# Kernel tuning notes

Measured on AMD Instinct MI355X. Metric: run time of the kernel, lower is better.

Reference implementation:

```python
import jax, jax.numpy as jnp
import numpy as np

B, T, D_MODEL = 1, 4096, 1024
H = 16
SEM_DIM, GEO_DIM, ATTN_DIM = 128, 256, 512
SEM_HD, GEO_HD, V_HD = SEM_DIM // H, GEO_DIM // H, ATTN_DIM // H
ROPE_BASE = 10000.0


def _split_heads(x, hd):
    # (B,T,H*hd) -> (B,H,T,hd)
    b, t, _ = x.shape
    return x.reshape(b, t, H, hd).transpose(0, 2, 1, 3)


def _rope(x, pos_offset, base=ROPE_BASE):
    # x: (B,H,T,rot) with rot == full geo head dim (rotate applies to first rot_dim;
    # here rot_dim == geo_head_dim so the whole vector rotates)
    rot = x.shape[-1]
    inv_freq = 1.0 / (base ** (jnp.arange(0, rot, 2, dtype=jnp.float32) / rot))
    t = jnp.arange(pos_offset, pos_offset + x.shape[2], dtype=jnp.float32)
    freqs = t[:, None] * inv_freq[None, :]            # (T, rot/2)
    cos = jnp.cos(freqs).astype(x.dtype)[None, None]  # (1,1,T,rot/2)
    sin = jnp.sin(freqs).astype(x.dtype)[None, None]
    x1, x2 = x[..., : rot // 2], x[..., rot // 2 :]
    return jnp.concatenate([x1 * cos - x2 * sin, x1 * sin + x2 * cos], axis=-1)


def setup_inputs() -> dict:
    key = jax.random.key(0)
    ks = jax.random.split(key, 8)
    s = lambda fan_in: 1.0 / np.sqrt(fan_in)
    inp = {
        "x": jax.random.normal(ks[0], (B, T, D_MODEL), dtype=jnp.float32),
        "q_sem_w": jax.random.uniform(ks[1], (SEM_DIM, D_MODEL), jnp.float32, -s(D_MODEL), s(D_MODEL)),
        "k_sem_w": jax.random.uniform(ks[2], (SEM_DIM, D_MODEL), jnp.float32, -s(D_MODEL), s(D_MODEL)),
        "q_geo_w": jax.random.uniform(ks[3], (GEO_DIM, D_MODEL), jnp.float32, -s(D_MODEL), s(D_MODEL)),
        "k_geo_w": jax.random.uniform(ks[4], (GEO_DIM, D_MODEL), jnp.float32, -s(D_MODEL), s(D_MODEL)),
        "v_w": jax.random.uniform(ks[5], (ATTN_DIM, D_MODEL), jnp.float32, -s(D_MODEL), s(D_MODEL)),
        "out_w": jax.random.uniform(ks[6], (D_MODEL, ATTN_DIM), jnp.float32, -s(ATTN_DIM), s(ATTN_DIM)),
        "logit_scale": jnp.zeros((H,), dtype=jnp.float32),
        "attn_mask": jnp.tril(jnp.ones((T, T), dtype=bool)),  # causal: True = attend
        "pos_offset": 0,
    }
    return inp


def reference(x, q_sem_w, k_sem_w, q_geo_w, k_geo_w, v_w, out_w, logit_scale, attn_mask, pos_offset):
    dt = x.dtype
    ninf = jnp.finfo(dt).min
    # decoupled projections
    qs = _split_heads(x @ q_sem_w.T, SEM_HD)   # (B,H,T,sem_hd)
    ksem = _split_heads(x @ k_sem_w.T, SEM_HD)
    qg = _split_heads(x @ q_geo_w.T, GEO_HD)   # (B,H,T,geo_hd)
    kg = _split_heads(x @ k_geo_w.T, GEO_HD)
    v = _split_heads(x @ v_w.T, V_HD)          # (B,H,T,v_hd)
    # RoPE on geometric stream only
    qg = _rope(qg, pos_offset)
    kg = _rope(kg, pos_offset)
    # combined scores, scaled as one concatenated QK dot product
    scale = 1.0 / np.sqrt(SEM_HD + GEO_HD)
    scores = (jnp.einsum("bhtd,bhsd->bhts", qs, ksem)
              + jnp.einsum("bhtd,bhsd->bhts", qg, kg)) * scale
    # learned per-head temperature
    scores = scores * jnp.exp(logit_scale)[None, :, None, None]
    scores = jnp.where(attn_mask[None, None], scores, ninf)
    attn = jax.nn.softmax(scores, axis=-1)
    out = jnp.einsum("bhts,bhsd->bhtd", attn, v)       # (B,H,T,v_hd)
    out = out.transpose(0, 2, 1, 3).reshape(B, T, ATTN_DIM)
    return out @ out_w.T                                # (B,T,d_model)
```

## Files before the change

kernel.cpp:

```cpp
#include <hip/hip_runtime.h>
#include <hip/hip_bf16.h>

typedef __attribute__((ext_vector_type(8))) short short8;
typedef __attribute__((ext_vector_type(4))) short short4v;
typedef __attribute__((ext_vector_type(4))) float f32x4;

#define TT 4096
#define DM 1024
#define NH 16
#define NPROJ 1280
#define DATTN 512

static __device__ __forceinline__ short f2bf(float f) {
  __hip_bfloat16 h = __float2bfloat16(f);
  return *reinterpret_cast<short*>(&h);
}
static __device__ __forceinline__ float bf2f(__hip_bfloat16 h) { return __bfloat162float(h); }
static __device__ __forceinline__ float bfs2f(short s) {
  __hip_bfloat16 h = *reinterpret_cast<__hip_bfloat16*>(&s);
  return __bfloat162float(h);
}

#define NB_X   (TT * DM / 4 / 256)
#define NB_OW  (DM * DATTN / 4 / 256)
#define NB_WC  (NPROJ * DM / 4 / 256)
__global__ __launch_bounds__(256) void k_prep(const float* __restrict__ x,
    const float* __restrict__ ow, const float* __restrict__ qs, const float* __restrict__ ks,
    const float* __restrict__ qg, const float* __restrict__ kg, const float* __restrict__ vw,
    __hip_bfloat16* __restrict__ Xbf, __hip_bfloat16* __restrict__ OW,
    __hip_bfloat16* __restrict__ Wcat) {
  const int b = blockIdx.x;
  if (b < NB_X) {
    const int i = b * 256 + threadIdx.x;
    float4 v = reinterpret_cast<const float4*>(x)[i];
    short4v o;
    o[0] = f2bf(v.x); o[1] = f2bf(v.y); o[2] = f2bf(v.z); o[3] = f2bf(v.w);
    reinterpret_cast<short4v*>(Xbf)[i] = o;
  } else if (b < NB_X + NB_OW) {
    const int i = (b - NB_X) * 256 + threadIdx.x;
    float4 v = reinterpret_cast<const float4*>(ow)[i];
    short4v o;
    o[0] = f2bf(v.x); o[1] = f2bf(v.y); o[2] = f2bf(v.z); o[3] = f2bf(v.w);
    reinterpret_cast<short4v*>(OW)[i] = o;
  } else {
    const int i = (b - NB_X - NB_OW) * 256 + threadIdx.x;
    const int idx = i * 4;
    const int row = idx >> 10;
    const int col = idx & 1023;
    const float* src;
    if (row < 128)      src = qs + (size_t)row * DM;
    else if (row < 256) src = ks + (size_t)(row - 128) * DM;
    else if (row < 512) src = qg + (size_t)(row - 256) * DM;
    else if (row < 768) src = kg + (size_t)(row - 512) * DM;
    else                src = vw + (size_t)(row - 768) * DM;
    float4 v = *reinterpret_cast<const float4*>(src + col);
    short4v o;
    o[0] = f2bf(v.x); o[1] = f2bf(v.y); o[2] = f2bf(v.z); o[3] = f2bf(v.w);
    *reinterpret_cast<short4v*>(Wcat + idx) = o;
  }
}

template<int OUT_BF16>
__global__ __launch_bounds__(256) void k_gemm_bt(const __hip_bfloat16* __restrict__ A,
    const __hip_bfloat16* __restrict__ B, void* __restrict__ Cv, int M, int N, int K) {
  __shared__ alignas(16) __hip_bfloat16 lA[64 * 32];
  __shared__ alignas(16) __hip_bfloat16 lB[128 * 32];
  const int tid = threadIdx.x;
  const int lane = tid & 63;
  const int wid = tid >> 6;
  const int m0 = blockIdx.x * 64, n0 = blockIdx.y * 128;
  const int wm = (wid >> 1) * 32, wn = (wid & 1) * 64;
  const int srow = tid >> 2;
  const int scol = (tid & 3) * 8;
  const int fr = lane & 15, fk = (lane >> 4) * 8;
  f32x4 acc[2][4];
  const f32x4 zz = {0.f, 0.f, 0.f, 0.f};
#pragma unroll
  for (int m = 0; m < 2; ++m)
#pragma unroll
    for (int n = 0; n < 4; ++n) acc[m][n] = zz;

  for (int kt = 0; kt < K; kt += 32) {
    __syncthreads();
    {
      const __hip_bfloat16* ga0 = A + (size_t)(m0 + srow) * K + kt + scol;
      const __hip_bfloat16* gb0 = B + (size_t)(n0 + srow) * K + kt + scol;
      const __hip_bfloat16* gb1 = B + (size_t)(n0 + 64 + srow) * K + kt + scol;
      __builtin_amdgcn_global_load_lds((const __attribute__((address_space(1))) void*)ga0,
          (__attribute__((address_space(3))) void*)(lA + srow * 32 + scol), 16, 0, 0);
      __builtin_amdgcn_global_load_lds((const __attribute__((address_space(1))) void*)gb0,
          (__attribute__((address_space(3))) void*)(lB + srow * 32 + scol), 16, 0, 0);
      __builtin_amdgcn_global_load_lds((const __attribute__((address_space(1))) void*)gb1,
          (__attribute__((address_space(3))) void*)(lB + (64 + srow) * 32 + scol), 16, 0, 0);
    }
    __syncthreads();
    short8 af[2], bfr[4];
#pragma unroll
    for (int m = 0; m < 2; ++m)
      af[m] = *reinterpret_cast<const short8*>(lA + (wm + m * 16 + fr) * 32 + fk);
#pragma unroll
    for (int n = 0; n < 4; ++n)
      bfr[n] = *reinterpret_cast<const short8*>(lB + (wn + n * 16 + fr) * 32 + fk);
#pragma unroll
    for (int m = 0; m < 2; ++m)
#pragma unroll
      for (int n = 0; n < 4; ++n)
        acc[m][n] = __builtin_amdgcn_mfma_f32_16x16x32_bf16(af[m], bfr[n], acc[m][n], 0, 0, 0);
  }
  const int cr = (lane >> 4) * 4, cc = lane & 15;
#pragma unroll
  for (int m = 0; m < 2; ++m)
#pragma unroll
    for (int n = 0; n < 4; ++n)
#pragma unroll
      for (int j = 0; j < 4; ++j) {
        const int row = m0 + wm + m * 16 + cr + j;
        const int col = n0 + wn + n * 16 + cc;
        if (OUT_BF16)
          ((__hip_bfloat16*)Cv)[(size_t)row * N + col] = __float2bfloat16(acc[m][n][j]);
        else
          ((float*)Cv)[(size_t)row * N + col] = acc[m][n][j];
      }
}

__global__ __launch_bounds__(256) void k_rope_pack(const __hip_bfloat16* __restrict__ proj,
    const float* __restrict__ ls, const int* __restrict__ posp,
    __hip_bfloat16* __restrict__ Qp, __hip_bfloat16* __restrict__ Kp,
    __hip_bfloat16* __restrict__ Vt) {
  const int gid = blockIdx.x * blockDim.x + threadIdx.x;
  const int t = gid & (TT - 1);
  const int h = gid >> 12;
  const short8* pr8 = reinterpret_cast<const short8*>(proj + (size_t)t * NPROJ);
  const short8 qs8 = pr8[h];
  const short8 ks8 = pr8[16 + h];
  const short8 qg1 = pr8[32 + 2 * h], qg2 = pr8[33 + 2 * h];
  const short8 kg1 = pr8[64 + 2 * h], kg2 = pr8[65 + 2 * h];
  const short8 vv0 = pr8[96 + 4 * h], vv1 = pr8[97 + 4 * h];
  const short8 vv2 = pr8[98 + 4 * h], vv3 = pr8[99 + 4 * h];
  const float qscale = 0.20412414523193154f * 1.4426950408889634f * __expf(ls[h]);
  const float pos = (float)(t + posp[0]);
  const float invf[8] = {1.0f, 0.31622776601683794f, 0.1f, 0.031622776601683794f,
                         0.01f, 0.0031622776601683794f, 0.001f, 0.00031622776601683794f};
  short8 qv[4], kv[4];
  const short8 z8 = {0, 0, 0, 0, 0, 0, 0, 0};
  qv[3] = z8; kv[3] = z8;
#pragma unroll
  for (int i = 0; i < 8; ++i) {
    qv[0][i] = f2bf(bfs2f(qs8[i]) * qscale);
    kv[0][i] = ks8[i];
  }
#pragma unroll
  for (int i = 0; i < 8; ++i) {
    const float ang = pos * invf[i];
    float ss, cc;
    __sincosf(ang, &ss, &cc);
    const float x1q = bfs2f(qg1[i]), x2q = bfs2f(qg2[i]);
    const float x1k = bfs2f(kg1[i]), x2k = bfs2f(kg2[i]);
    qv[1][i] = f2bf((x1q * cc - x2q * ss) * qscale);
    qv[2][i] = f2bf((x1q * ss + x2q * cc) * qscale);
    kv[1][i] = f2bf(x1k * cc - x2k * ss);
    kv[2][i] = f2bf(x1k * ss + x2k * cc);
  }
  short8* qdst = reinterpret_cast<short8*>(Qp + ((size_t)h * TT + t) * 32);
  short8* kdst = reinterpret_cast<short8*>(Kp + ((size_t)h * TT + t) * 32);
#pragma unroll
  for (int p = 0; p < 4; ++p) { qdst[p] = qv[p]; kdst[p] = kv[p]; }
  __hip_bfloat16* vdst = Vt + (size_t)h * 32 * TT + t;
#pragma unroll
  for (int i = 0; i < 8; ++i) {
    *reinterpret_cast<short*>(vdst + (size_t)i * TT) = vv0[i];
    *reinterpret_cast<short*>(vdst + (size_t)(8 + i) * TT) = vv1[i];
    *reinterpret_cast<short*>(vdst + (size_t)(16 + i) * TT) = vv2[i];
    *reinterpret_cast<short*>(vdst + (size_t)(24 + i) * TT) = vv3[i];
  }
}

__global__ __launch_bounds__(256) void k_attn(const __hip_bfloat16* __restrict__ Qp,
    const __hip_bfloat16* __restrict__ Kp, const __hip_bfloat16* __restrict__ Vt,
    __hip_bfloat16* __restrict__ Ob) {
  __shared__ alignas(16) __hip_bfloat16 lK[2][64 * 32];
  __shared__ alignas(16) __hip_bfloat16 lV[2][32 * 64];
  __shared__ alignas(16) __hip_bfloat16 Plds[4][16][72];
  const int lin = blockIdx.x;
  const int xcd = lin & 7;
  const int idx = lin >> 3;
  const int h = xcd * 2 + (idx & 1);
  const int qb = 63 - (idx >> 1);
  const int nt = qb + 1;
  const int tid = threadIdx.x;
  const int lane = tid & 63, w = tid >> 6;
  const int g = lane >> 4, c = lane & 15;
  const int krow = (tid >> 6) * 16 + (tid & 15);
  const int kcol = ((tid >> 4) & 3) * 8;
  const int vrow = ((tid >> 6) & 1) * 16 + (tid & 15);
  const int vcol = ((tid >> 7) & 1) * 32 + ((tid >> 4) & 3) * 8;
  const __hip_bfloat16* Kh = Kp + (size_t)h * TT * 32 + (size_t)krow * 32 + kcol;
  const __hip_bfloat16* Vh = Vt + (size_t)h * 32 * TT + (size_t)vrow * TT + vcol;
  const f32x4 zz = {0.f, 0.f, 0.f, 0.f};

  const int qrow = qb * 64 + w * 16 + c;
  const short8 qf =
      *reinterpret_cast<const short8*>(Qp + ((size_t)h * TT + qrow) * 32 + 8 * g);
  f32x4 o0 = zz, o1 = zz;
  float mst = -1e30f, lsum = 0.f;
  int cur = 0;
  __builtin_amdgcn_global_load_lds(
      (const __attribute__((address_space(1))) void*)Kh,
      (__attribute__((address_space(3))) void*)(lK[0] + tid * 8), 16, 0, 0);
  __builtin_amdgcn_global_load_lds(
      (const __attribute__((address_space(1))) void*)Vh,
      (__attribute__((address_space(3))) void*)(lV[0] + tid * 8), 16, 0, 0);

  for (int it = 0; it < nt; ++it) {
    __syncthreads();
    if (it + 1 < nt) {
      const int kv1 = (it + 1) * 64;
      __builtin_amdgcn_global_load_lds(
          (const __attribute__((address_space(1))) void*)(Kh + (size_t)kv1 * 32),
          (__attribute__((address_space(3))) void*)(lK[cur ^ 1] + tid * 8), 16, 0, 0);
      __builtin_amdgcn_global_load_lds(
          (const __attribute__((address_space(1))) void*)(Vh + kv1),
          (__attribute__((address_space(3))) void*)(lV[cur ^ 1] + tid * 8), 16, 0, 0);
    }
    const char* kb = (const char*)lK[cur];
    short8 kf[4];
#pragma unroll
    for (int ct = 0; ct < 4; ++ct)
      kf[ct] = *reinterpret_cast<const short8*>(kb + ct * 1024 + lane * 16);
    const char* vb = (const char*)lV[cur];
    const short8 v00 = *reinterpret_cast<const short8*>(vb + lane * 16);
    const short8 v10 = *reinterpret_cast<const short8*>(vb + 1024 + lane * 16);
    const short8 v01 = *reinterpret_cast<const short8*>(vb + 2048 + lane * 16);
    const short8 v11 = *reinterpret_cast<const short8*>(vb + 3072 + lane * 16);
    f32x4 s[4];
#pragma unroll
    for (int ct = 0; ct < 4; ++ct)
      s[ct] = __builtin_amdgcn_mfma_f32_16x16x32_bf16(kf[ct], qf, zz, 0, 0, 0);
    if (it == nt - 1) {
#pragma unroll
      for (int ct = 0; ct < 4; ++ct)
#pragma unroll
        for (int j = 0; j < 4; ++j)
          if (ct * 16 + g * 4 + j > w * 16 + c) s[ct][j] = -1e30f;
    }
    float m01 = fmaxf(fmaxf(s[0][0], s[0][1]), fmaxf(s[0][2], s[0][3]));
    float m23 = fmaxf(fmaxf(s[1][0], s[1][1]), fmaxf(s[1][2], s[1][3]));
    float m45 = fmaxf(fmaxf(s[2][0], s[2][1]), fmaxf(s[2][2], s[2][3]));
    float m67 = fmaxf(fmaxf(s[3][0], s[3][1]), fmaxf(s[3][2], s[3][3]));
    float pm_ = fmaxf(fmaxf(m01, m23), fmaxf(m45, m67));
    if (__any(pm_ > mst + 8.0f)) {
      float pm2 = fmaxf(pm_, __shfl_xor(pm_, 16, 64));
      pm2 = fmaxf(pm2, __shfl_xor(pm2, 32, 64));
      const float nm = fmaxf(mst, pm2);
      const float alpha = exp2f(mst - nm);
      mst = nm;
      lsum *= alpha;
#pragma unroll
      for (int j = 0; j < 4; ++j) { o0[j] *= alpha; o1[j] *= alpha; }
    }
    float ts = 0.f;
#pragma unroll
    for (int ct = 0; ct < 4; ++ct) {
#pragma unroll
      for (int j = 0; j < 4; ++j) s[ct][j] = exp2f(s[ct][j] - mst);
      ts += (s[ct][0] + s[ct][1]) + (s[ct][2] + s[ct][3]);
    }
    lsum += ts;
#pragma unroll
    for (int ct = 0; ct < 4; ++ct) {
      float2 p01; p01.x = s[ct][0]; p01.y = s[ct][1];
      float2 p23; p23.x = s[ct][2]; p23.y = s[ct][3];
      __hip_bfloat162 b01 = __float22bfloat162_rn(p01);
      __hip_bfloat162 b23 = __float22bfloat162_rn(p23);
      *reinterpret_cast<__hip_bfloat162*>(&Plds[w][c][ct * 16 + g * 4]) = b01;
      *reinterpret_cast<__hip_bfloat162*>(&Plds[w][c][ct * 16 + g * 4 + 2]) = b23;
    }
    const short8 pf0 = *reinterpret_cast<const short8*>(&Plds[w][c][8 * g]);
    const short8 pf1 = *reinterpret_cast<const short8*>(&Plds[w][c][32 + 8 * g]);
    o0 = __builtin_amdgcn_mfma_f32_16x16x32_bf16(v00, pf0, o0, 0, 0, 0);
    o0 = __builtin_amdgcn_mfma_f32_16x16x32_bf16(v01, pf1, o0, 0, 0, 0);
    o1 = __builtin_amdgcn_mfma_f32_16x16x32_bf16(v10, pf0, o1, 0, 0, 0);
    o1 = __builtin_amdgcn_mfma_f32_16x16x32_bf16(v11, pf1, o1, 0, 0, 0);
    cur ^= 1;
  }
  lsum += __shfl_xor(lsum, 16, 64);
  lsum += __shfl_xor(lsum, 32, 64);
  const float inv = 1.0f / lsum;
  __hip_bfloat16* dst = Ob + (size_t)qrow * DATTN + h * 32;
  short4v w0, w1;
#pragma unroll
  for (int j = 0; j < 4; ++j) { w0[j] = f2bf(o0[j] * inv); w1[j] = f2bf(o1[j] * inv); }
  *reinterpret_cast<short4v*>(dst + g * 4) = w0;
  *reinterpret_cast<short4v*>(dst + 16 + g * 4) = w1;
}

extern "C" void kernel_launch(void* const* d_in, const int* in_sizes, int n_in,
                              void* d_out, int out_size, void* d_ws, size_t ws_size,
                              hipStream_t stream) {
  const float* x   = (const float*)d_in[0];
  const float* qsw = (const float*)d_in[1];
  const float* ksw = (const float*)d_in[2];
  const float* qgw = (const float*)d_in[3];
  const float* kgw = (const float*)d_in[4];
  const float* vw  = (const float*)d_in[5];
  const float* ow  = (const float*)d_in[6];
  const float* ls  = (const float*)d_in[7];
  const int* posp  = (const int*)d_in[9];

  size_t off = 0;
  auto alloc = [&](size_t bytes) {
    char* p = (char*)d_ws + off;
    off += (bytes + 255) & ~(size_t)255;
    return (void*)p;
  };
  __hip_bfloat16* Xbf  = (__hip_bfloat16*)alloc((size_t)TT * DM * 2);
  __hip_bfloat16* Wcat = (__hip_bfloat16*)alloc((size_t)NPROJ * DM * 2);
  __hip_bfloat16* OW   = (__hip_bfloat16*)alloc((size_t)DM * DATTN * 2);
  __hip_bfloat16* proj = (__hip_bfloat16*)alloc((size_t)TT * NPROJ * 2);
  __hip_bfloat16* Qp   = (__hip_bfloat16*)alloc((size_t)NH * TT * 32 * 2);
  __hip_bfloat16* Kpk  = (__hip_bfloat16*)alloc((size_t)NH * TT * 32 * 2);
  __hip_bfloat16* Vt   = (__hip_bfloat16*)alloc((size_t)NH * 32 * TT * 2);
  __hip_bfloat16* Ob   = (__hip_bfloat16*)alloc((size_t)TT * DATTN * 2);

  k_prep<<<dim3(NB_X + NB_OW + NB_WC), 256, 0, stream>>>(x, ow, qsw, ksw, qgw, kgw, vw,
                                                         Xbf, OW, Wcat);
  k_gemm_bt<1><<<dim3(TT / 64, NPROJ / 128), 256, 0, stream>>>(Xbf, Wcat, (void*)proj,
                                                               TT, NPROJ, DM);
  k_rope_pack<<<dim3(TT * NH / 256), 256, 0, stream>>>(proj, ls, posp, Qp, Kpk, Vt);
  k_attn<<<dim3(1024), 256, 0, stream>>>(Qp, Kpk, Vt, Ob);
  k_gemm_bt<0><<<dim3(TT / 64, DM / 128), 256, 0, stream>>>(Ob, OW, (void*)d_out,
                                                            TT, DM, DATTN);
}
```

Before: 122.3 us.

## Double-buffer GEMM LDS tiles and process 128 queries per attention block

The GEMM kernel now double-buffers its LDS tiles so the next K-slice is prefetched while the current one feeds MFMA, which removes one barrier per iteration. The attention kernel gives each wave two 16-row query fragments (128 queries per block, 512 blocks). Each K/V tile loaded into LDS is therefore reused across twice as many queries, halving K/V traffic per query. The cost is more registers per wave and fewer blocks, which may lower occupancy and worsen load balance on the causal triangle.

After: 152.1 us. 1.24x slower.

```diff
diff --git a/kernel.cpp b/kernel.cpp
--- a/kernel.cpp
+++ b/kernel.cpp
@@ -15,7 +15,6 @@
   __hip_bfloat16 h = __float2bfloat16(f);
   return *reinterpret_cast<short*>(&h);
 }
-static __device__ __forceinline__ float bf2f(__hip_bfloat16 h) { return __bfloat162float(h); }
 static __device__ __forceinline__ float bfs2f(short s) {
   __hip_bfloat16 h = *reinterpret_cast<__hip_bfloat16*>(&s);
   return __bfloat162float(h);
@@ -63,8 +62,8 @@
 template<int OUT_BF16>
 __global__ __launch_bounds__(256) void k_gemm_bt(const __hip_bfloat16* __restrict__ A,
     const __hip_bfloat16* __restrict__ B, void* __restrict__ Cv, int M, int N, int K) {
-  __shared__ alignas(16) __hip_bfloat16 lA[64 * 32];
-  __shared__ alignas(16) __hip_bfloat16 lB[128 * 32];
+  __shared__ alignas(16) __hip_bfloat16 lA[2][64 * 32];
+  __shared__ alignas(16) __hip_bfloat16 lB[2][128 * 32];
   const int tid = threadIdx.x;
   const int lane = tid & 63;
   const int wid = tid >> 6;
@@ -80,32 +79,35 @@
 #pragma unroll
     for (int n = 0; n < 4; ++n) acc[m][n] = zz;
 
+  auto stage = [&](int kt, int buf) {
+    const __hip_bfloat16* ga0 = A + (size_t)(m0 + srow) * K + kt + scol;
+    const __hip_bfloat16* gb0 = B + (size_t)(n0 + srow) * K + kt + scol;
+    const __hip_bfloat16* gb1 = B + (size_t)(n0 + 64 + srow) * K + kt + scol;
+    __builtin_amdgcn_global_load_lds((const __attribute__((address_space(1))) void*)ga0,
+        (__attribute__((address_space(3))) void*)(lA[buf] + srow * 32 + scol), 16, 0, 0);
+    __builtin_amdgcn_global_load_lds((const __attribute__((address_space(1))) void*)gb0,
+        (__attribute__((address_space(3))) void*)(lB[buf] + srow * 32 + scol), 16, 0, 0);
+    __builtin_amdgcn_global_load_lds((const __attribute__((address_space(1))) void*)gb1,
+        (__attribute__((address_space(3))) void*)(lB[buf] + (64 + srow) * 32 + scol), 16, 0, 0);
+  };
+  stage(0, 0);
+  int buf = 0;
   for (int kt = 0; kt < K; kt += 32) {
     __syncthreads();
-    {
-      const __hip_bfloat16* ga0 = A + (size_t)(m0 + srow) * K + kt + scol;
-      const __hip_bfloat16* gb0 = B + (size_t)(n0 + srow) * K + kt + scol;
-      const __hip_bfloat16* gb1 = B + (size_t)(n0 + 64 + srow) * K + kt + scol;
-      __builtin_amdgcn_global_load_lds((const __attribute__((address_space(1))) void*)ga0,
-          (__attribute__((address_space(3))) void*)(lA + srow * 32 + scol), 16, 0, 0);
-      __builtin_amdgcn_global_load_lds((const __attribute__((address_space(1))) void*)gb0,
-          (__attribute__((address_space(3))) void*)(lB + srow * 32 + scol), 16, 0, 0);
-      __builtin_amdgcn_global_load_lds((const __attribute__((address_space(1))) void*)gb1,
-          (__attribute__((address_space(3))) void*)(lB + (64 + srow) * 32 + scol), 16, 0, 0);
-    }
-    __syncthreads();
+    if (kt + 32 < K) stage(kt + 32, buf ^ 1);
     short8 af[2], bfr[4];
 #pragma unroll
     for (int m = 0; m < 2; ++m)
-      af[m] = *reinterpret_cast<const short8*>(lA + (wm + m * 16 + fr) * 32 + fk);
+      af[m] = *reinterpret_cast<const short8*>(lA[buf] + (wm + m * 16 + fr) * 32 + fk);
 #pragma unroll
     for (int n = 0; n < 4; ++n)
-      bfr[n] = *reinterpret_cast<const short8*>(lB + (wn + n * 16 + fr) * 32 + fk);
+      bfr[n] = *reinterpret_cast<const short8*>(lB[buf] + (wn + n * 16 + fr) * 32 + fk);
 #pragma unroll
     for (int m = 0; m < 2; ++m)
 #pragma unroll
       for (int n = 0; n < 4; ++n)
         acc[m][n] = __builtin_amdgcn_mfma_f32_16x16x32_bf16(af[m], bfr[n], acc[m][n], 0, 0, 0);
+    buf ^= 1;
   }
   const int cr = (lane >> 4) * 4, cc = lane & 15;
 #pragma unroll
@@ -180,13 +182,14 @@
     __hip_bfloat16* __restrict__ Ob) {
   __shared__ alignas(16) __hip_bfloat16 lK[2][64 * 32];
   __shared__ alignas(16) __hip_bfloat16 lV[2][32 * 64];
-  __shared__ alignas(16) __hip_bfloat16 Plds[4][16][72];
+  __shared__ alignas(16) __hip_bfloat16 Plds[4][2][16][72];
   const int lin = blockIdx.x;
   const int xcd = lin & 7;
   const int idx = lin >> 3;
   const int h = xcd * 2 + (idx & 1);
-  const int qb = 63 - (idx >> 1);
-  const int nt = qb + 1;
+  const int qb = 31 - (idx >> 1);
+  const int nt = 2 * qb + 2;
+  const int base = qb * 128;
   const int tid = threadIdx.x;
   const int lane = tid & 63, w = tid >> 6;
   const int g = lane >> 4, c = lane & 15;
@@ -198,11 +201,14 @@
   const __hip_bfloat16* Vh = Vt + (size_t)h * 32 * TT + (size_t)vrow * TT + vcol;
   const f32x4 zz = {0.f, 0.f, 0.f, 0.f};
 
-  const int qrow = qb * 64 + w * 16 + c;
-  const short8 qf =
-      *reinterpret_cast<const short8*>(Qp + ((size_t)h * TT + qrow) * 32 + 8 * g);
-  f32x4 o0 = zz, o1 = zz;
-  float mst = -1e30f, lsum = 0.f;
+  const int q0 = base + w * 32 + c;
+  const int q1 = q0 + 16;
+  const short8 qf0 =
+      *reinterpret_cast<const short8*>(Qp + ((size_t)h * TT + q0) * 32 + 8 * g);
+  const short8 qf1 =
+      *reinterpret_cast<const short8*>(Qp + ((size_t)h * TT + q1) * 32 + 8 * g);
+  f32x4 o00 = zz, o01 = zz, o10 = zz, o11 = zz;
+  float mst0 = -1e30f, ls0 = 0.f, mst1 = -1e30f, ls1 = 0.f;
   int cur = 0;
   __builtin_amdgcn_global_load_lds(
       (const __attribute__((address_space(1))) void*)Kh,
@@ -232,66 +238,119 @@
     const short8 v10 = *reinterpret_cast<const short8*>(vb + 1024 + lane * 16);
     const short8 v01 = *reinterpret_cast<const short8*>(vb + 2048 + lane * 16);
     const short8 v11 = *reinterpret_cast<const short8*>(vb + 3072 + lane * 16);
-    f32x4 s[4];
-#pragma unroll
-    for (int ct = 0; ct < 4; ++ct)
-      s[ct] = __builtin_amdgcn_mfma_f32_16x16x32_bf16(kf[ct], qf, zz, 0, 0, 0);
-    if (it == nt - 1) {
+    f32x4 s0[4], s1[4];
+#pragma unroll
+    for (int ct = 0; ct < 4; ++ct) {
+      s0[ct] = __builtin_amdgcn_mfma_f32_16x16x32_bf16(kf[ct], qf0, zz, 0, 0, 0);
+      s1[ct] = __builtin_amdgcn_mfma_f32_16x16x32_bf16(kf[ct], qf1, zz, 0, 0, 0);
+    }
+    if (it >= nt - 2) {
+      const int kv0 = it * 64;
 #pragma unroll
       for (int ct = 0; ct < 4; ++ct)
 #pragma unroll
-        for (int j = 0; j < 4; ++j)
-          if (ct * 16 + g * 4 + j > w * 16 + c) s[ct][j] = -1e30f;
-    }
-    float m01 = fmaxf(fmaxf(s[0][0], s[0][1]), fmaxf(s[0][2], s[0][3]));
-    float m23 = fmaxf(fmaxf(s[1][0], s[1][1]), fmaxf(s[1][2], s[1][3]));
-    float m45 = fmaxf(fmaxf(s[2][0], s[2][1]), fmaxf(s[2][2], s[2][3]));
-    float m67 = fmaxf(fmaxf(s[3][0], s[3][1]), fmaxf(s[3][2], s[3][3]));
-    float pm_ = fmaxf(fmaxf(m01, m23), fmaxf(m45, m67));
-    if (__any(pm_ > mst + 8.0f)) {
-      float pm2 = fmaxf(pm_, __shfl_xor(pm_, 16, 64));
-      pm2 = fmaxf(pm2, __shfl_xor(pm2, 32, 64));
-      const float nm = fmaxf(mst, pm2);
-      const float alpha = exp2f(mst - nm);
-      mst = nm;
-      lsum *= alpha;
-#pragma unroll
-      for (int j = 0; j < 4; ++j) { o0[j] *= alpha; o1[j] *= alpha; }
-    }
-    float ts = 0.f;
+        for (int j = 0; j < 4; ++j) {
+          const int kvi = kv0 + ct * 16 + g * 4 + j;
+          if (kvi > q0) s0[ct][j] = -1e30f;
+          if (kvi > q1) s1[ct][j] = -1e30f;
+        }
+    }
+    {
+      float m01 = fmaxf(fmaxf(s0[0][0], s0[0][1]), fmaxf(s0[0][2], s0[0][3]));
+      float m23 = fmaxf(fmaxf(s0[1][0], s0[1][1]), fmaxf(s0[1][2], s0[1][3]));
+      float m45 = fmaxf(fmaxf(s0[2][0], s0[2][1]), fmaxf(s0[2][2], s0[2][3]));
+      float m67 = fmaxf(fmaxf(s0[3][0], s0[3][1]), fmaxf(s0[3][2], s0[3][3]));
+      float pm_ = fmaxf(fmaxf(m01, m23), fmaxf(m45, m67));
+      if (__any(pm_ > mst0 + 8.0f)) {
+        float pm2 = fmaxf(pm_, __shfl_xor(pm_, 16, 64));
+        pm2 = fmaxf(pm2, __shfl_xor(pm2, 32, 64));
+        const float nm = fmaxf(mst0, pm2);
+        const float alpha = exp2f(mst0 - nm);
+        mst0 = nm;
+        ls0 *= alpha;
+#pragma unroll
+        for (int j = 0; j < 4; ++j) { o00[j] *= alpha; o01[j] *= alpha; }
+      }
+      float ts = 0.f;
+#pragma unroll
+      for (int ct = 0; ct < 4; ++ct) {
+#pragma unroll
+        for (int j = 0; j < 4; ++j) s0[ct][j] = exp2f(s0[ct][j] - mst0);
+        ts += (s0[ct][0] + s0[ct][1]) + (s0[ct][2] + s0[ct][3]);
+      }
+      ls0 += ts;
+    }
+    {
+      float m01 = fmaxf(fmaxf(s1[0][0], s1[0][1]), fmaxf(s1[0][2], s1[0][3]));
+      float m23 = fmaxf(fmaxf(s1[1][0], s1[1][1]), fmaxf(s1[1][2], s1[1][3]));
+      float m45 = fmaxf(fmaxf(s1[2][0], s1[2][1]), fmaxf(s1[2][2], s1[2][3]));
+      float m67 = fmaxf(fmaxf(s1[3][0], s1[3][1]), fmaxf(s1[3][2], s1[3][3]));
+      float pm_ = fmaxf(fmaxf(m01, m23), fmaxf(m45, m67));
+      if (__any(pm_ > mst1 + 8.0f)) {
+        float pm2 = fmaxf(pm_, __shfl_xor(pm_, 16, 64));
+        pm2 = fmaxf(pm2, __shfl_xor(pm2, 32, 64));
+        const float nm = fmaxf(mst1, pm2);
+        const float alpha = exp2f(mst1 - nm);
+        mst1 = nm;
+        ls1 *= alpha;
+#pragma unroll
+        for (int j = 0; j < 4; ++j) { o10[j] *= alpha; o11[j] *= alpha; }
+      }
+      float ts = 0.f;
+#pragma unroll
+      for (int ct = 0; ct < 4; ++ct) {
+#pragma unroll
+        for (int j = 0; j < 4; ++j) s1[ct][j] = exp2f(s1[ct][j] - mst1);
+        ts += (s1[ct][0] + s1[ct][1]) + (s1[ct][2] + s1[ct][3]);
+      }
+      ls1 += ts;
+    }
 #pragma unroll
     for (int ct = 0; ct < 4; ++ct) {
-#pragma unroll
-      for (int j = 0; j < 4; ++j) s[ct][j] = exp2f(s[ct][j] - mst);
-      ts += (s[ct][0] + s[ct][1]) + (s[ct][2] + s[ct][3]);
-    }
-    lsum += ts;
-#pragma unroll
-    for (int ct = 0; ct < 4; ++ct) {
-      float2 p01; p01.x = s[ct][0]; p01.y = s[ct][1];
-      float2 p23; p23.x = s[ct][2]; p23.y = s[ct][3];
-      __hip_bfloat162 b01 = __float22bfloat162_rn(p01);
-      __hip_bfloat162 b23 = __float22bfloat162_rn(p23);
-      *reinterpret_cast<__hip_bfloat162*>(&Plds[w][c][ct * 16 + g * 4]) = b01;
-      *reinterpret_cast<__hip_bfloat162*>(&Plds[w][c][ct * 16 + g * 4 + 2]) = b23;
-    }
-    const short8 pf0 = *reinterpret_cast<const short8*>(&Plds[w][c][8 * g]);
-    const short8 pf1 = *reinterpret_cast<const short8*>(&Plds[w][c][32 + 8 * g]);
-    o0 = __builtin_amdgcn_mfma_f32_16x16x32_bf16(v00, pf0, o0, 0, 0, 0);
-    o0 = __builtin_amdgcn_mfma_f32_16x16x32_bf16(v01, pf1, o0, 0, 0, 0);
-    o1 = __builtin_amdgcn_mfma_f32_16x16x32_bf16(v10, pf0, o1, 0, 0, 0);
-    o1 = __builtin_amdgcn_mfma_f32_16x16x32_bf16(v11, pf1, o1, 0, 0, 0);
+      float2 a01; a01.x = s0[ct][0]; a01.y = s0[ct][1];
+      float2 a23; a23.x = s0[ct][2]; a23.y = s0[ct][3];
+      __hip_bfloat162 b01 = __float22bfloat162_rn(a01);
+      __hip_bfloat162 b23 = __float22bfloat162_rn(a23);
+      *reinterpret_cast<__hip_bfloat162*>(&Plds[w][0][c][ct * 16 + g * 4]) = b01;
+      *reinterpret_cast<__hip_bfloat162*>(&Plds[w][0][c][ct * 16 + g * 4 + 2]) = b23;
+      float2 d01; d01.x = s1[ct][0]; d01.y = s1[ct][1];
+      float2 d23; d23.x = s1[ct][2]; d23.y = s1[ct][3];
+      __hip_bfloat162 e01 = __float22bfloat162_rn(d01);
+      __hip_bfloat162 e23 = __float22bfloat162_rn(d23);
+      *reinterpret_cast<__hip_bfloat162*>(&Plds[w][1][c][ct * 16 + g * 4]) = e01;
+      *reinterpret_cast<__hip_bfloat162*>(&Plds[w][1][c][ct * 16 + g * 4 + 2]) = e23;
+    }
+    const short8 p00 = *reinterpret_cast<const short8*>(&Plds[w][0][c][8 * g]);
+    const short8 p01 = *reinterpret_cast<const short8*>(&Plds[w][0][c][32 + 8 * g]);
+    const short8 p10 = *reinterpret_cast<const short8*>(&Plds[w][1][c][8 * g]);
+    const short8 p11 = *reinterpret_cast<const short8*>(&Plds[w][1][c][32 + 8 * g]);
+    o00 = __builtin_amdgcn_mfma_f32_16x16x32_bf16(v00, p00, o00, 0, 0, 0);
+    o00 = __builtin_amdgcn_mfma_f32_16x16x32_bf16(v01, p01, o00, 0, 0, 0);
+    o01 = __builtin_amdgcn_mfma_f32_16x16x32_bf16(v10, p00, o01, 0, 0, 0);
+    o01 = __builtin_amdgcn_mfma_f32_16x16x32_bf16(v11, p01, o01, 0, 0, 0);
+    o10 = __builtin_amdgcn_mfma_f32_16x16x32_bf16(v00, p10, o10, 0, 0, 0);
+    o10 = __builtin_amdgcn_mfma_f32_16x16x32_bf16(v01, p11, o10, 0, 0, 0);
+    o11 = __builtin_amdgcn_mfma_f32_16x16x32_bf16(v10, p10, o11, 0, 0, 0);
+    o11 = __builtin_amdgcn_mfma_f32_16x16x32_bf16(v11, p11, o11, 0, 0, 0);
     cur ^= 1;
   }
-  lsum += __shfl_xor(lsum, 16, 64);
-  lsum += __shfl_xor(lsum, 32, 64);
-  const float inv = 1.0f / lsum;
-  __hip_bfloat16* dst = Ob + (size_t)qrow * DATTN + h * 32;
-  short4v w0, w1;
-#pragma unroll
-  for (int j = 0; j < 4; ++j) { w0[j] = f2bf(o0[j] * inv); w1[j] = f2bf(o1[j] * inv); }
-  *reinterpret_cast<short4v*>(dst + g * 4) = w0;
-  *reinterpret_cast<short4v*>(dst + 16 + g * 4) = w1;
+  ls0 += __shfl_xor(ls0, 16, 64);
+  ls0 += __shfl_xor(ls0, 32, 64);
+  ls1 += __shfl_xor(ls1, 16, 64);
+  ls1 += __shfl_xor(ls1, 32, 64);
+  const float inv0 = 1.0f / ls0, inv1 = 1.0f / ls1;
+  __hip_bfloat16* dst0 = Ob + (size_t)q0 * DATTN + h * 32;
+  __hip_bfloat16* dst1 = Ob + (size_t)q1 * DATTN + h * 32;
+  short4v w00, w01, w10, w11;
+#pragma unroll
+  for (int j = 0; j < 4; ++j) {
+    w00[j] = f2bf(o00[j] * inv0); w01[j] = f2bf(o01[j] * inv0);
+    w10[j] = f2bf(o10[j] * inv1); w11[j] = f2bf(o11[j] * inv1);
+  }
+  *reinterpret_cast<short4v*>(dst0 + g * 4) = w00;
+  *reinterpret_cast<short4v*>(dst0 + 16 + g * 4) = w01;
+  *reinterpret_cast<short4v*>(dst1 + g * 4) = w10;
+  *reinterpret_cast<short4v*>(dst1 + 16 + g * 4) = w11;
 }
 
 extern "C" void kernel_launch(void* const* d_in, const int* in_sizes, int n_in,
@@ -327,7 +386,7 @@
   k_gemm_bt<1><<<dim3(TT / 64, NPROJ / 128), 256, 0, stream>>>(Xbf, Wcat, (void*)proj,
                                                                TT, NPROJ, DM);
   k_rope_pack<<<dim3(TT * NH / 256), 256, 0, stream>>>(proj, ls, posp, Qp, Kpk, Vt);
-  k_attn<<<dim3(1024), 256, 0, stream>>>(Qp, Kpk, Vt, Ob);
+  k_attn<<<dim3(512), 256, 0, stream>>>(Qp, Kpk, Vt, Ob);
   k_gemm_bt<0><<<dim3(TT / 64, DM / 128), 256, 0, stream>>>(Ob, OW, (void*)d_out,
                                                             TT, DM, DATTN);
 }
```

## Split attention KV tile across wave pairs and double-buffer GEMM LDS staging

Applied to the files above, without the earlier changes.

The attention kernel now gives each wave 32 query rows and half of each 64-key tile, rather than 16 query rows over all 64 keys. The P matrix stays in registers as the MFMA B operand instead of going through an LDS round-trip. Partial softmax states from each wave pair are merged through LDS in an epilogue. The projection GEMM gains double-buffered LDS so the next K-slice load overlaps the current MFMAs, which removes one barrier per iteration; this doubles LDS use and adds an epilogue reduction to attention.

After: 122.9 us. Within noise of the previous version (+0.6%).

```diff
diff --git a/kernel.cpp b/kernel.cpp
--- a/kernel.cpp
+++ b/kernel.cpp
@@ -15,10 +15,14 @@
   __hip_bfloat16 h = __float2bfloat16(f);
   return *reinterpret_cast<short*>(&h);
 }
-static __device__ __forceinline__ float bf2f(__hip_bfloat16 h) { return __bfloat162float(h); }
 static __device__ __forceinline__ float bfs2f(short s) {
   __hip_bfloat16 h = *reinterpret_cast<__hip_bfloat16*>(&s);
   return __bfloat162float(h);
+}
+static __device__ __forceinline__ unsigned pk2(float a, float b) {
+  float2 t; t.x = a; t.y = b;
+  __hip_bfloat162 r = __float22bfloat162_rn(t);
+  return *reinterpret_cast<unsigned*>(&r);
 }
 
 #define NB_X   (TT * DM / 4 / 256)
@@ -63,8 +67,8 @@
 template<int OUT_BF16>
 __global__ __launch_bounds__(256) void k_gemm_bt(const __hip_bfloat16* __restrict__ A,
     const __hip_bfloat16* __restrict__ B, void* __restrict__ Cv, int M, int N, int K) {
-  __shared__ alignas(16) __hip_bfloat16 lA[64 * 32];
-  __shared__ alignas(16) __hip_bfloat16 lB[128 * 32];
+  __shared__ alignas(16) __hip_bfloat16 lA[2][64 * 32];
+  __shared__ alignas(16) __hip_bfloat16 lB[2][128 * 32];
   const int tid = threadIdx.x;
   const int lane = tid & 63;
   const int wid = tid >> 6;
@@ -80,32 +84,35 @@
 #pragma unroll
     for (int n = 0; n < 4; ++n) acc[m][n] = zz;
 
+  auto stage = [&](int kt, int buf) {
+    const __hip_bfloat16* ga0 = A + (size_t)(m0 + srow) * K + kt + scol;
+    const __hip_bfloat16* gb0 = B + (size_t)(n0 + srow) * K + kt + scol;
+    const __hip_bfloat16* gb1 = B + (size_t)(n0 + 64 + srow) * K + kt + scol;
+    __builtin_amdgcn_global_load_lds((const __attribute__((address_space(1))) void*)ga0,
+        (__attribute__((address_space(3))) void*)(lA[buf] + srow * 32 + scol), 16, 0, 0);
+    __builtin_amdgcn_global_load_lds((const __attribute__((address_space(1))) void*)gb0,
+        (__attribute__((address_space(3))) void*)(lB[buf] + srow * 32 + scol), 16, 0, 0);
+    __builtin_amdgcn_global_load_lds((const __attribute__((address_space(1))) void*)gb1,
+        (__attribute__((address_space(3))) void*)(lB[buf] + (64 + srow) * 32 + scol), 16, 0, 0);
+  };
+  stage(0, 0);
+  int buf = 0;
   for (int kt = 0; kt < K; kt += 32) {
     __syncthreads();
-    {
-      const __hip_bfloat16* ga0 = A + (size_t)(m0 + srow) * K + kt + scol;
-      const __hip_bfloat16* gb0 = B + (size_t)(n0 + srow) * K + kt + scol;
-      const __hip_bfloat16* gb1 = B + (size_t)(n0 + 64 + srow) * K + kt + scol;
-      __builtin_amdgcn_global_load_lds((const __attribute__((address_space(1))) void*)ga0,
-          (__attribute__((address_space(3))) void*)(lA + srow * 32 + scol), 16, 0, 0);
-      __builtin_amdgcn_global_load_lds((const __attribute__((address_space(1))) void*)gb0,
-          (__attribute__((address_space(3))) void*)(lB + srow * 32 + scol), 16, 0, 0);
-      __builtin_amdgcn_global_load_lds((const __attribute__((address_space(1))) void*)gb1,
-          (__attribute__((address_space(3))) void*)(lB + (64 + srow) * 32 + scol), 16, 0, 0);
-    }
-    __syncthreads();
+    if (kt + 32 < K) stage(kt + 32, buf ^ 1);
     short8 af[2], bfr[4];
 #pragma unroll
     for (int m = 0; m < 2; ++m)
-      af[m] = *reinterpret_cast<const short8*>(lA + (wm + m * 16 + fr) * 32 + fk);
+      af[m] = *reinterpret_cast<const short8*>(lA[buf] + (wm + m * 16 + fr) * 32 + fk);
 #pragma unroll
     for (int n = 0; n < 4; ++n)
-      bfr[n] = *reinterpret_cast<const short8*>(lB + (wn + n * 16 + fr) * 32 + fk);
+      bfr[n] = *reinterpret_cast<const short8*>(lB[buf] + (wn + n * 16 + fr) * 32 + fk);
 #pragma unroll
     for (int m = 0; m < 2; ++m)
 #pragma unroll
       for (int n = 0; n < 4; ++n)
         acc[m][n] = __builtin_amdgcn_mfma_f32_16x16x32_bf16(af[m], bfr[n], acc[m][n], 0, 0, 0);
+    buf ^= 1;
   }
   const int cr = (lane >> 4) * 4, cc = lane & 15;
 #pragma unroll
@@ -180,7 +187,8 @@
     __hip_bfloat16* __restrict__ Ob) {
   __shared__ alignas(16) __hip_bfloat16 lK[2][64 * 32];
   __shared__ alignas(16) __hip_bfloat16 lV[2][32 * 64];
-  __shared__ alignas(16) __hip_bfloat16 Plds[4][16][72];
+  __shared__ alignas(16) f32x4 Olds[4][2][2][4][16];
+  __shared__ float Mlds[4][2][16], Llds[4][2][16];
   const int lin = blockIdx.x;
   const int xcd = lin & 7;
   const int idx = lin >> 3;
@@ -189,7 +197,9 @@
   const int nt = qb + 1;
   const int tid = threadIdx.x;
   const int lane = tid & 63, w = tid >> 6;
+  const int qh = w >> 1, kh = w & 1;
   const int g = lane >> 4, c = lane & 15;
+  const float NINF = -__builtin_inff();
   const int krow = (tid >> 6) * 16 + (tid & 15);
   const int kcol = ((tid >> 4) & 3) * 8;
   const int vrow = ((tid >> 6) & 1) * 16 + (tid & 15);
@@ -197,12 +207,17 @@
   const __hip_bfloat16* Kh = Kp + (size_t)h * TT * 32 + (size_t)krow * 32 + kcol;
   const __hip_bfloat16* Vh = Vt + (size_t)h * 32 * TT + (size_t)vrow * TT + vcol;
   const f32x4 zz = {0.f, 0.f, 0.f, 0.f};
-
-  const int qrow = qb * 64 + w * 16 + c;
-  const short8 qf =
-      *reinterpret_cast<const short8*>(Qp + ((size_t)h * TT + qrow) * 32 + 8 * g);
-  f32x4 o0 = zz, o1 = zz;
-  float mst = -1e30f, lsum = 0.f;
+  const int vb0 = kh * 2048 + (g >> 1) * 256 + c * 16 + 8 * (g & 1);
+
+  const int qbase = qb * 64 + 32 * qh;
+  short8 qf[2];
+#pragma unroll
+  for (int f = 0; f < 2; ++f)
+    qf[f] = *reinterpret_cast<const short8*>(Qp + ((size_t)h * TT + qbase + 16 * f + c) * 32 + 8 * g);
+  f32x4 o[2][2];
+  o[0][0] = zz; o[0][1] = zz; o[1][0] = zz; o[1][1] = zz;
+  float mst[2] = {-1e30f, -1e30f};
+  float lsum[2] = {0.f, 0.f};
   int cur = 0;
   __builtin_amdgcn_global_load_lds(
       (const __attribute__((address_space(1))) void*)Kh,
@@ -223,75 +238,97 @@
           (__attribute__((address_space(3))) void*)(lV[cur ^ 1] + tid * 8), 16, 0, 0);
     }
     const char* kb = (const char*)lK[cur];
-    short8 kf[4];
-#pragma unroll
-    for (int ct = 0; ct < 4; ++ct)
-      kf[ct] = *reinterpret_cast<const short8*>(kb + ct * 1024 + lane * 16);
+    short8 kf[2];
+#pragma unroll
+    for (int ct = 0; ct < 2; ++ct)
+      kf[ct] = *reinterpret_cast<const short8*>(kb + (2 * kh + ct) * 1024 + lane * 16);
     const char* vb = (const char*)lV[cur];
-    const short8 v00 = *reinterpret_cast<const short8*>(vb + lane * 16);
-    const short8 v10 = *reinterpret_cast<const short8*>(vb + 1024 + lane * 16);
-    const short8 v01 = *reinterpret_cast<const short8*>(vb + 2048 + lane * 16);
-    const short8 v11 = *reinterpret_cast<const short8*>(vb + 3072 + lane * 16);
-    f32x4 s[4];
-#pragma unroll
-    for (int ct = 0; ct < 4; ++ct)
-      s[ct] = __builtin_amdgcn_mfma_f32_16x16x32_bf16(kf[ct], qf, zz, 0, 0, 0);
+    union U8 { unsigned u[4]; short8 v8; };
+    U8 aV[2];
+#pragma unroll
+    for (int db = 0; db < 2; ++db) {
+      *reinterpret_cast<uint2*>(&aV[db].u[0]) =
+          *reinterpret_cast<const uint2*>(vb + vb0 + db * 1024);
+      *reinterpret_cast<uint2*>(&aV[db].u[2]) =
+          *reinterpret_cast<const uint2*>(vb + vb0 + db * 1024 + 512);
+    }
+    f32x4 s[2][2];
+#pragma unroll
+    for (int f = 0; f < 2; ++f)
+#pragma unroll
+      for (int ct = 0; ct < 2; ++ct)
+        s[f][ct] = __builtin_amdgcn_mfma_f32_16x16x32_bf16(kf[ct], qf[f], zz, 0, 0, 0);
     if (it == nt - 1) {
 #pragma unroll
-      for (int ct = 0; ct < 4; ++ct)
-#pragma unroll
-        for (int j = 0; j < 4; ++j)
-          if (ct * 16 + g * 4 + j > w * 16 + c) s[ct][j] = -1e30f;
-    }
-    float m01 = fmaxf(fmaxf(s[0][0], s[0][1]), fmaxf(s[0][2], s[0][3]));
-    float m23 = fmaxf(fmaxf(s[1][0], s[1][1]), fmaxf(s[1][2], s[1][3]));
-    float m45 = fmaxf(fmaxf(s[2][0], s[2][1]), fmaxf(s[2][2], s[2][3]));
-    float m67 = fmaxf(fmaxf(s[3][0], s[3][1]), fmaxf(s[3][2], s[3][3]));
-    float pm_ = fmaxf(fmaxf(m01, m23), fmaxf(m45, m67));
-    if (__any(pm_ > mst + 8.0f)) {
-      float pm2 = fmaxf(pm_, __shfl_xor(pm_, 16, 64));
-      pm2 = fmaxf(pm2, __shfl_xor(pm2, 32, 64));
-      const float nm = fmaxf(mst, pm2);
-      const float alpha = exp2f(mst - nm);
-      mst = nm;
-      lsum *= alpha;
-#pragma unroll
-      for (int j = 0; j < 4; ++j) { o0[j] *= alpha; o1[j] *= alpha; }
-    }
-    float ts = 0.f;
-#pragma unroll
-    for (int ct = 0; ct < 4; ++ct) {
-#pragma unroll
-      for (int j = 0; j < 4; ++j) s[ct][j] = exp2f(s[ct][j] - mst);
-      ts += (s[ct][0] + s[ct][1]) + (s[ct][2] + s[ct][3]);
-    }
-    lsum += ts;
-#pragma unroll
-    for (int ct = 0; ct < 4; ++ct) {
-      float2 p01; p01.x = s[ct][0]; p01.y = s[ct][1];
-      float2 p23; p23.x = s[ct][2]; p23.y = s[ct][3];
-      __hip_bfloat162 b01 = __float22bfloat162_rn(p01);
-      __hip_bfloat162 b23 = __float22bfloat162_rn(p23);
-      *reinterpret_cast<__hip_bfloat162*>(&Plds[w][c][ct * 16 + g * 4]) = b01;
-      *reinterpret_cast<__hip_bfloat162*>(&Plds[w][c][ct * 16 + g * 4 + 2]) = b23;
-    }
-    const short8 pf0 = *reinterpret_cast<const short8*>(&Plds[w][c][8 * g]);
-    const short8 pf1 = *reinterpret_cast<const short8*>(&Plds[w][c][32 + 8 * g]);
-    o0 = __builtin_amdgcn_mfma_f32_16x16x32_bf16(v00, pf0, o0, 0, 0, 0);
-    o0 = __builtin_amdgcn_mfma_f32_16x16x32_bf16(v01, pf1, o0, 0, 0, 0);
-    o1 = __builtin_amdgcn_mfma_f32_16x16x32_bf16(v10, pf0, o1, 0, 0, 0);
-    o1 = __builtin_amdgcn_mfma_f32_16x16x32_bf16(v11, pf1, o1, 0, 0, 0);
+      for (int f = 0; f < 2; ++f)
+#pragma unroll
+        for (int ct = 0; ct < 2; ++ct)
+#pragma unroll
+          for (int j = 0; j < 4; ++j)
+            if (32 * kh + 16 * ct + 4 * g + j > 32 * qh + 16 * f + c) s[f][ct][j] = NINF;
+    }
+#pragma unroll
+    for (int f = 0; f < 2; ++f) {
+      float a = fmaxf(fmaxf(s[f][0][0], s[f][0][1]), fmaxf(s[f][0][2], s[f][0][3]));
+      float b = fmaxf(fmaxf(s[f][1][0], s[f][1][1]), fmaxf(s[f][1][2], s[f][1][3]));
+      float pm_ = fmaxf(a, b);
+      if (__any(pm_ > mst[f] + 8.0f)) {
+        float pm2 = fmaxf(pm_, __shfl_xor(pm_, 16, 64));
+        pm2 = fmaxf(pm2, __shfl_xor(pm2, 32, 64));
+        const float nm = fmaxf(mst[f], pm2);
+        const float alpha = exp2f(mst[f] - nm);
+        mst[f] = nm;
+        lsum[f] *= alpha;
+#pragma unroll
+        for (int j = 0; j < 4; ++j) { o[f][0][j] *= alpha; o[f][1][j] *= alpha; }
+      }
+      float ts = 0.f;
+#pragma unroll
+      for (int ct = 0; ct < 2; ++ct) {
+#pragma unroll
+        for (int j = 0; j < 4; ++j) s[f][ct][j] = exp2f(s[f][ct][j] - mst[f]);
+        ts += (s[f][ct][0] + s[f][ct][1]) + (s[f][ct][2] + s[f][ct][3]);
+      }
+      lsum[f] += ts;
+      U8 pb;
+      pb.u[0] = pk2(s[f][0][0], s[f][0][1]);
+      pb.u[1] = pk2(s[f][0][2], s[f][0][3]);
+      pb.u[2] = pk2(s[f][1][0], s[f][1][1]);
+      pb.u[3] = pk2(s[f][1][2], s[f][1][3]);
+      o[f][0] = __builtin_amdgcn_mfma_f32_16x16x32_bf16(aV[0].v8, pb.v8, o[f][0], 0, 0, 0);
+      o[f][1] = __builtin_amdgcn_mfma_f32_16x16x32_bf16(aV[1].v8, pb.v8, o[f][1], 0, 0, 0);
+    }
     cur ^= 1;
   }
-  lsum += __shfl_xor(lsum, 16, 64);
-  lsum += __shfl_xor(lsum, 32, 64);
-  const float inv = 1.0f / lsum;
-  __hip_bfloat16* dst = Ob + (size_t)qrow * DATTN + h * 32;
-  short4v w0, w1;
-#pragma unroll
-  for (int j = 0; j < 4; ++j) { w0[j] = f2bf(o0[j] * inv); w1[j] = f2bf(o1[j] * inv); }
-  *reinterpret_cast<short4v*>(dst + g * 4) = w0;
-  *reinterpret_cast<short4v*>(dst + 16 + g * 4) = w1;
+#pragma unroll
+  for (int f = 0; f < 2; ++f) {
+    lsum[f] += __shfl_xor(lsum[f], 16, 64);
+    lsum[f] += __shfl_xor(lsum[f], 32, 64);
+#pragma unroll
+    for (int db = 0; db < 2; ++db) Olds[w][f][db][g][c] = o[f][db];
+    if (g == 0) { Mlds[w][f][c] = mst[f]; Llds[w][f][c] = lsum[f]; }
+  }
+  __syncthreads();
+  {
+    const int ql = tid >> 2, dq = tid & 3;
+    const int mqh = ql >> 5, mf = (ql >> 4) & 1, mc = ql & 15;
+    const int w0 = 2 * mqh, w1 = w0 + 1;
+    const int db = dq >> 1, gp = (dq & 1) * 2;
+    const float m0 = Mlds[w0][mf][mc], m1 = Mlds[w1][mf][mc];
+    const float mm = fmaxf(m0, m1);
+    const float e0 = exp2f(m0 - mm), e1 = exp2f(m1 - mm);
+    const float inv = 1.0f / (Llds[w0][mf][mc] * e0 + Llds[w1][mf][mc] * e1);
+    const f32x4 a0 = Olds[w0][mf][db][gp][mc], a1 = Olds[w0][mf][db][gp + 1][mc];
+    const f32x4 b0 = Olds[w1][mf][db][gp][mc], b1 = Olds[w1][mf][db][gp + 1][mc];
+    short8 ov;
+#pragma unroll
+    for (int j = 0; j < 4; ++j) {
+      ov[j] = f2bf((a0[j] * e0 + b0[j] * e1) * inv);
+      ov[4 + j] = f2bf((a1[j] * e0 + b1[j] * e1) * inv);
+    }
+    const int qrow = qb * 64 + ql;
+    *reinterpret_cast<short8*>(Ob + (size_t)qrow * DATTN + h * 32 + db * 16 + gp * 4) = ov;
+  }
 }
 
 extern "C" void kernel_launch(void* const* d_in, const int* in_sizes, int n_in,
```
